# Optimization experiments

Measured on AMD Instinct MI355X. Metric: run time of the kernel, lower is better.

## Reference

```python
import jax, jax.numpy as jnp
import numpy as np

N_NODES = 100000
N_EDGES = 1280000
D_IN = 64
D_HID = 64
D_OUT = 1
N_GRAPHS = 512


def setup_inputs() -> dict:
    key = jax.random.key(0)
    ks = jax.random.split(key, 12)
    x = jax.random.normal(ks[0], (N_NODES, D_IN), dtype=jnp.float32)
    edge_index = jax.random.randint(ks[1], (2, N_EDGES), 0, N_NODES, dtype=jnp.int32)
    batch = jnp.sort(jax.random.randint(ks[2], (N_NODES,), 0, N_GRAPHS, dtype=jnp.int32))
    s = 0.1
    w0 = jax.random.normal(ks[3], (D_IN, D_HID), dtype=jnp.float32) * s
    b0 = jnp.zeros((D_HID,), dtype=jnp.float32)
    w1 = jax.random.normal(ks[4], (D_HID, D_HID), dtype=jnp.float32) * s
    b1 = jnp.zeros((D_HID,), dtype=jnp.float32)
    w2 = jax.random.normal(ks[5], (D_HID, D_HID), dtype=jnp.float32) * s
    b2 = jnp.zeros((D_HID,), dtype=jnp.float32)
    fc_w = jax.random.normal(ks[6], (D_HID, D_OUT), dtype=jnp.float32) * s
    fc_b = jnp.zeros((D_OUT,), dtype=jnp.float32)
    return {"x": x, "edge_index": edge_index, "batch": batch,
            "w0": w0, "b0": b0, "w1": w1, "b1": b1, "w2": w2, "b2": b2,
            "fc_w": fc_w, "fc_b": fc_b}


def _gcn_conv(x, w, b, src, dst):
    # PyG GCNConv: h = x @ W; out_i = sum_j norm_ij * h_j over (A + I), sym norm.
    h = x @ w                                           # [N, H]
    ones = jnp.ones((src.shape[0],), dtype=h.dtype)
    deg = jax.ops.segment_sum(ones, dst, num_segments=N_NODES) + 1.0  # +1 self-loop
    dinv = jax.lax.rsqrt(deg)                           # [N]
    norm = dinv[src] * dinv[dst]                        # [E]
    agg = jax.ops.segment_sum(h[src] * norm[:, None], dst, num_segments=N_NODES)
    agg = agg + h * (dinv * dinv)[:, None]              # self-loop term
    return agg + b


def reference(x, edge_index, batch, w0, b0, w1, b1, w2, b2, fc_w, fc_b):
    src, dst = edge_index[0], edge_index[1]
    # 3 stacked GCNConv + relu (dropout is identity in eval mode)
    h = jax.nn.relu(_gcn_conv(x, w0, b0, src, dst))
    h = jax.nn.relu(_gcn_conv(h, w1, b1, src, dst))
    h = jax.nn.relu(_gcn_conv(h, w2, b2, src, dst))
    # global mean pool per graph
    sums = jax.ops.segment_sum(h, batch, num_segments=N_GRAPHS)        # [G, H]
    cnt = jax.ops.segment_sum(jnp.ones((N_NODES,), h.dtype), batch, num_segments=N_GRAPHS)
    mean = sums / jnp.maximum(cnt, 1.0)[:, None]
    return mean @ fc_w + fc_b                            # [G, 1]
```

## Files before the change

kernel.cpp:

```cpp
#include <hip/hip_runtime.h>
#include <hip/hip_fp16.h>
#include <type_traits>

#define N_NODES 100000
#define N_EDGES 1280000
#define N_GRAPHS 512
#define NBK 196
#define CHUNK 3200
#define NCH 400
#define CAP 8192

typedef _Float16 v8h __attribute__((ext_vector_type(8)));
typedef float v4f __attribute__((ext_vector_type(4)));

__device__ inline void fmix_lo(float& acc, unsigned h2, float n) {
    asm volatile("v_fma_mix_f32 %0, %1, %2, %0 op_sel:[0,0,0] op_sel_hi:[1,0,0]"
                 : "+v"(acc) : "v"(h2), "v"(n));
}
__device__ inline void fmix_hi(float& acc, unsigned h2, float n) {
    asm volatile("v_fma_mix_f32 %0, %1, %2, %0 op_sel:[1,0,0] op_sel_hi:[1,0,0]"
                 : "+v"(acc) : "v"(h2), "v"(n));
}


__global__ __launch_bounds__(256) void edge_scatter(const int* __restrict__ src,
                                                    const int* __restrict__ dst,
                                                    int* __restrict__ bcur,
                                                    int2* __restrict__ pairs) {
    __shared__ int2 buf[CHUNK];
    __shared__ int lcnt[NBK], lloc[NBK], lcur[NBK];
    __shared__ int s[256];
    int t = threadIdx.x;
    for (int k = t; k < NBK; k += 256) { lcnt[k] = 0; lcur[k] = 0; }
    __syncthreads();
    int e0 = blockIdx.x * CHUNK;
    for (int i = t; i < CHUNK; i += 256) atomicAdd(&lcnt[dst[e0 + i] >> 9], 1);
    __syncthreads();
    {
        int v = (t < NBK) ? lcnt[t] : 0;
        s[t] = v; __syncthreads();
        for (int d = 1; d < 256; d <<= 1) {
            int x = (t >= d) ? s[t - d] : 0;
            __syncthreads();
            s[t] += x;
            __syncthreads();
        }
        if (t < NBK) lloc[t] = s[t] - v;
    }
    __syncthreads();
    for (int i = t; i < CHUNK; i += 256) {
        int d = dst[e0 + i];
        int k = d >> 9;
        int li = lloc[k] + atomicAdd(&lcur[k], 1);
        buf[li] = make_int2(src[e0 + i], d);
    }
    __syncthreads();
    for (int k = t; k < NBK; k += 256) {
        int c = lcnt[k];
        if (c) {
            int g = atomicAdd(&bcur[k * 16], c);
            int lo = lloc[k];
            int2* dstp = pairs + (size_t)k * CAP;
            for (int j = 0; j < c; j++)
                if (g + j < CAP) dstp[g + j] = buf[lo + j];
        }
    }
}


__global__ void bucket_scan(const int* __restrict__ bcur, int* __restrict__ bbase,
                            int* __restrict__ offs) {
    __shared__ int s[256];
    int t = threadIdx.x;
    int v = (t < NBK) ? min(bcur[t * 16], CAP) : 0;
    s[t] = v; __syncthreads();
    for (int d = 1; d < 256; d <<= 1) {
        int x = (t >= d) ? s[t - d] : 0;
        __syncthreads();
        s[t] += x;
        __syncthreads();
    }
    if (t < NBK) bbase[t] = s[t] - v;
    if (t == 0) offs[N_NODES] = N_EDGES;
}


__global__ __launch_bounds__(512) void bucket_place(const int2* __restrict__ pairs,
                                                    const int* __restrict__ bbase,
                                                    const int* __restrict__ bcur,
                                                    int* __restrict__ offs,
                                                    float* __restrict__ dinv,
                                                    int* __restrict__ csr) {
    __shared__ int lcnt[512];
    __shared__ int lofs[512];
    __shared__ int lcur[512];
    __shared__ int lsrc[CAP];
    int t = threadIdx.x;
    int b = blockIdx.x;
    int node0 = b << 9;
    int nn = min(512, N_NODES - node0);
    int beg = bbase[b];
    int cnt = min(bcur[b * 16], CAP);
    const int2* prs = pairs + (size_t)b * CAP;
    lcnt[t] = 0; lcur[t] = 0;
    __syncthreads();
    for (int i = t; i < cnt; i += 512)
        atomicAdd(&lcnt[prs[i].y - node0], 1);
    __syncthreads();
    int deg = lcnt[t];
    for (int d = 1; d < 512; d <<= 1) {
        int x = (t >= d) ? lcnt[t - d] : 0;
        __syncthreads();
        lcnt[t] += x;
        __syncthreads();
    }
    lofs[t] = lcnt[t] - deg;
    if (t < nn) {
        offs[node0 + t] = beg + lcnt[t] - deg;
        dinv[node0 + t] = 1.0f / sqrtf((float)deg + 1.0f);
    }
    __syncthreads();
    for (int i = t; i < cnt; i += 512) {
        int2 pr = prs[i];
        int n = pr.y - node0;
        int li = lofs[n] + atomicAdd(&lcur[n], 1);
        if (li < CAP) lsrc[li] = pr.x;
    }
    __syncthreads();
    for (int j = t; j < cnt; j += 512) csr[beg + j] = lsrc[j];
}


template <typename T>
__global__ __launch_bounds__(256) void gemm_mfma(const T* __restrict__ X,
                                                 const float* __restrict__ W,
                                                 __half* __restrict__ H) {
    __shared__ _Float16 Wt[64][72];
    int t = threadIdx.x;
    {
        #pragma unroll
        for (int q = 0; q < 4; q++) {
            int idx = t + q * 256;
            int k = idx >> 4;
            int n0 = (idx & 15) * 4;
            float4 v = ((const float4*)W)[idx];
            Wt[n0 + 0][k] = (_Float16)v.x;
            Wt[n0 + 1][k] = (_Float16)v.y;
            Wt[n0 + 2][k] = (_Float16)v.z;
            Wt[n0 + 3][k] = (_Float16)v.w;
        }
    }
    __syncthreads();

    int wv = t >> 6, lane = t & 63;
    int m = lane & 15, quad = lane >> 4;

    v8h bf[4][2];
    #pragma unroll
    for (int c = 0; c < 4; c++)
        #pragma unroll
        for (int h = 0; h < 2; h++)
            bf[c][h] = *(const v8h*)&Wt[c * 16 + m][h * 32 + quad * 8];

    int base = blockIdx.x * 256 + wv * 64;
    #pragma unroll
    for (int tt = 0; tt < 4; tt++) {
        int tile = base + tt * 16;
        int rA = min(tile + m, N_NODES - 1);
        v8h a0, a1;
        if constexpr (std::is_same<T, float>::value) {
            const float* xp = (const float*)X + (size_t)rA * 64 + quad * 8;
            float4 p0 = *(const float4*)xp;
            float4 p1 = *(const float4*)(xp + 4);
            float4 p2 = *(const float4*)(xp + 32);
            float4 p3 = *(const float4*)(xp + 36);
            a0 = (v8h){(_Float16)p0.x, (_Float16)p0.y, (_Float16)p0.z, (_Float16)p0.w,
                       (_Float16)p1.x, (_Float16)p1.y, (_Float16)p1.z, (_Float16)p1.w};
            a1 = (v8h){(_Float16)p2.x, (_Float16)p2.y, (_Float16)p2.z, (_Float16)p2.w,
                       (_Float16)p3.x, (_Float16)p3.y, (_Float16)p3.z, (_Float16)p3.w};
        } else {
            const _Float16* xp = (const _Float16*)X + (size_t)rA * 64 + quad * 8;
            a0 = *(const v8h*)xp;
            a1 = *(const v8h*)(xp + 32);
        }
        v4f acc[4];
        #pragma unroll
        for (int c = 0; c < 4; c++) {
            acc[c] = (v4f){0.f, 0.f, 0.f, 0.f};
            acc[c] = __builtin_amdgcn_mfma_f32_16x16x32_f16(a0, bf[c][0], acc[c], 0, 0, 0);
            acc[c] = __builtin_amdgcn_mfma_f32_16x16x32_f16(a1, bf[c][1], acc[c], 0, 0, 0);
        }
        #pragma unroll
        for (int r = 0; r < 4; r++) {
            int row = tile + quad * 4 + r;
            if (row < N_NODES) {
                __half* hp = H + (size_t)row * 64 + m;
                #pragma unroll
                for (int c = 0; c < 4; c++)
                    hp[c * 16] = __float2half(acc[c][r]);
            }
        }
    }
}


__device__ inline void agg_body(const uint2* __restrict__ Hh, int wid, int lane,
                                const int* __restrict__ offs,
                                const int* __restrict__ csr,
                                const float* __restrict__ dinv,
                                float4& out) {
    int eg = lane >> 4;
    int fq = lane & 15;
    int beg = offs[wid], end = offs[wid + 1];
    float di = dinv[wid];
    uint2 us = Hh[(size_t)wid * 16 + fq];

    float4 a0 = {0.f, 0.f, 0.f, 0.f};
    float4 a1 = {0.f, 0.f, 0.f, 0.f};
    for (int base = beg; base < end; base += 16) {
        int i0 = base + eg;
        int r0 = csr[i0], r1 = csr[i0 + 4], r2 = csr[i0 + 8], r3 = csr[i0 + 12];
        bool p0 = i0      < end, p1 = i0 + 4  < end,
             p2 = i0 + 8  < end, p3 = i0 + 12 < end;
        int s0 = p0 ? r0 : 0, s1 = p1 ? r1 : 0,
            s2 = p2 ? r2 : 0, s3 = p3 ? r3 : 0;
        uint2 u0 = Hh[(size_t)s0 * 16 + fq];
        uint2 u1 = Hh[(size_t)s1 * 16 + fq];
        uint2 u2 = Hh[(size_t)s2 * 16 + fq];
        uint2 u3 = Hh[(size_t)s3 * 16 + fq];
        float d0 = dinv[s0], d1 = dinv[s1], d2 = dinv[s2], d3 = dinv[s3];
        float n0 = p0 ? d0 * di : 0.f;
        float n1 = p1 ? d1 * di : 0.f;
        float n2 = p2 ? d2 * di : 0.f;
        float n3 = p3 ? d3 * di : 0.f;
        fmix_lo(a0.x, u0.x, n0); fmix_hi(a0.y, u0.x, n0);
        fmix_lo(a0.z, u0.y, n0); fmix_hi(a0.w, u0.y, n0);
        fmix_lo(a1.x, u1.x, n1); fmix_hi(a1.y, u1.x, n1);
        fmix_lo(a1.z, u1.y, n1); fmix_hi(a1.w, u1.y, n1);
        fmix_lo(a0.x, u2.x, n2); fmix_hi(a0.y, u2.x, n2);
        fmix_lo(a0.z, u2.y, n2); fmix_hi(a0.w, u2.y, n2);
        fmix_lo(a1.x, u3.x, n3); fmix_hi(a1.y, u3.x, n3);
        fmix_lo(a1.z, u3.y, n3); fmix_hi(a1.w, u3.y, n3);
    }
    a0.x += a1.x; a0.y += a1.y; a0.z += a1.z; a0.w += a1.w;
    a0.x += __shfl_xor(a0.x, 16); a0.y += __shfl_xor(a0.y, 16);
    a0.z += __shfl_xor(a0.z, 16); a0.w += __shfl_xor(a0.w, 16);
    a0.x += __shfl_xor(a0.x, 32); a0.y += __shfl_xor(a0.y, 32);
    a0.z += __shfl_xor(a0.z, 32); a0.w += __shfl_xor(a0.w, 32);
    float2 s01 = __half22float2(*(__half2*)&us.x);
    float2 s23 = __half22float2(*(__half2*)&us.y);
    float dd = di * di;
    out.x = a0.x + s01.x * dd; out.y = a0.y + s01.y * dd;
    out.z = a0.z + s23.x * dd; out.w = a0.w + s23.y * dd;
}

__global__ __launch_bounds__(256) void agg_gcn(const __half* __restrict__ H,
                                               const int* __restrict__ offs,
                                               const int* __restrict__ csr,
                                               const float* __restrict__ dinv,
                                               const float* __restrict__ bias,
                                               __half* __restrict__ Out) {
    int wid = (blockIdx.x * 256 + threadIdx.x) >> 6;
    int lane = threadIdx.x & 63;
    if (wid >= N_NODES) return;
    float4 r;
    agg_body((const uint2*)H, wid, lane, offs, csr, dinv, r);
    int fq = lane & 15;
    if ((lane >> 4) == 0) {
        float4 b4 = ((const float4*)bias)[fq];
        __half2 h01 = __float22half2_rn(make_float2(fmaxf(r.x + b4.x, 0.f),
                                                    fmaxf(r.y + b4.y, 0.f)));
        __half2 h23 = __float22half2_rn(make_float2(fmaxf(r.z + b4.z, 0.f),
                                                    fmaxf(r.w + b4.w, 0.f)));
        uint2 u;
        u.x = *(unsigned int*)&h01;
        u.y = *(unsigned int*)&h23;
        ((uint2*)Out)[(size_t)wid * 16 + fq] = u;
    }
}

__global__ __launch_bounds__(256) void agg_gcn_pool(const __half* __restrict__ H,
                                                    const int* __restrict__ offs,
                                                    const int* __restrict__ csr,
                                                    const float* __restrict__ dinv,
                                                    const float* __restrict__ bias,
                                                    const float* __restrict__ fcw,
                                                    float* __restrict__ p) {
    int wid = (blockIdx.x * 256 + threadIdx.x) >> 6;
    int lane = threadIdx.x & 63;
    if (wid >= N_NODES) return;
    float4 r;
    agg_body((const uint2*)H, wid, lane, offs, csr, dinv, r);
    int fq = lane & 15;
    float4 b4 = ((const float4*)bias)[fq];
    float4 f4 = ((const float4*)fcw)[fq];
    float v = fmaxf(r.x + b4.x, 0.f) * f4.x + fmaxf(r.y + b4.y, 0.f) * f4.y
            + fmaxf(r.z + b4.z, 0.f) * f4.z + fmaxf(r.w + b4.w, 0.f) * f4.w;
    v += __shfl_xor(v, 1); v += __shfl_xor(v, 2);
    v += __shfl_xor(v, 4); v += __shfl_xor(v, 8);
    if (lane == 0) p[wid] = v;
}


__device__ inline int lower_bound_batch(const int* __restrict__ batch, int key) {
    int lo = 0, hi = N_NODES;
    while (lo < hi) {
        int mid = (lo + hi) >> 1;
        if (batch[mid] < key) lo = mid + 1; else hi = mid;
    }
    return lo;
}

__global__ __launch_bounds__(256) void graph_reduce(const float* __restrict__ p,
                                                    const int* __restrict__ batch,
                                                    const float* __restrict__ fcb,
                                                    float* __restrict__ out) {
    __shared__ float red[4];
    int g = blockIdx.x;
    int s0 = lower_bound_batch(batch, g);
    int s1 = lower_bound_batch(batch, g + 1);
    float acc = 0.f;
    for (int i = s0 + threadIdx.x; i < s1; i += 256) acc += p[i];
    #pragma unroll
    for (int o = 32; o > 0; o >>= 1) acc += __shfl_xor(acc, o);
    int lane = threadIdx.x & 63, wv = threadIdx.x >> 6;
    if (lane == 0) red[wv] = acc;
    __syncthreads();
    if (threadIdx.x == 0) {
        float sum = red[0] + red[1] + red[2] + red[3];
        out[g] = sum / fmaxf((float)(s1 - s0), 1.f) + fcb[0];
    }
}


extern "C" void kernel_launch(void* const* d_in, const int* in_sizes, int n_in,
                              void* d_out, int out_size, void* d_ws, size_t ws_size,
                              hipStream_t stream) {
    const float* x    = (const float*)d_in[0];
    const int*   ei   = (const int*)d_in[1];
    const int*   batch= (const int*)d_in[2];
    const float* w0   = (const float*)d_in[3];
    const float* b0   = (const float*)d_in[4];
    const float* w1   = (const float*)d_in[5];
    const float* b1   = (const float*)d_in[6];
    const float* w2   = (const float*)d_in[7];
    const float* b2   = (const float*)d_in[8];
    const float* fcw  = (const float*)d_in[9];
    const float* fcb  = (const float*)d_in[10];
    float* out = (float*)d_out;

    const int* src_e = ei;
    const int* dst_e = ei + N_EDGES;

    char* w = (char*)d_ws;
    size_t o = 0;
    int*    bcur  = (int*)(w + o);    o += 256 * 16 * 4;
    int*    bbase = (int*)(w + o);    o += 256 * 4;
    int*    offs  = (int*)(w + o);    o += (size_t)(N_NODES + 8) * 4;
    float*  dinv  = (float*)(w + o);  o += (size_t)N_NODES * 4;
    int2*   pairs = (int2*)(w + o);   o += (size_t)NBK * CAP * 8;
    int*    csr   = (int*)(w + o);    o += (size_t)(N_EDGES + 16) * 4;
    __half* bufA  = (__half*)(w + o); o += (size_t)N_NODES * 64 * 2;
    __half* bufB  = (__half*)(w + o); o += (size_t)N_NODES * 64 * 2;
    float*  pvec  = (float*)(w + o);  o += (size_t)N_NODES * 4;

    hipMemsetAsync(bcur, 0, 256 * 16 * 4, stream);
    hipMemsetAsync(csr + N_EDGES, 0, 16 * 4, stream);

    edge_scatter<<<NCH, 256, 0, stream>>>(src_e, dst_e, bcur, pairs);
    bucket_scan<<<1, 256, 0, stream>>>(bcur, bbase, offs);
    bucket_place<<<NBK, 512, 0, stream>>>(pairs, bbase, bcur, offs, dinv, csr);

    const int GEMM_BLOCKS = (N_NODES + 255) / 256;
    const int AGG_BLOCKS  = (N_NODES + 3) / 4;

    gemm_mfma<float><<<GEMM_BLOCKS, 256, 0, stream>>>(x, w0, bufA);
    agg_gcn<<<AGG_BLOCKS, 256, 0, stream>>>(bufA, offs, csr, dinv, b0, bufB);

    gemm_mfma<__half><<<GEMM_BLOCKS, 256, 0, stream>>>(bufB, w1, bufA);
    agg_gcn<<<AGG_BLOCKS, 256, 0, stream>>>(bufA, offs, csr, dinv, b1, bufB);

    gemm_mfma<__half><<<GEMM_BLOCKS, 256, 0, stream>>>(bufB, w2, bufA);
    agg_gcn_pool<<<AGG_BLOCKS, 256, 0, stream>>>(bufA, offs, csr, dinv, b2, fcw, pvec);

    graph_reduce<<<N_GRAPHS, 256, 0, stream>>>(pvec, batch, fcb, out);
}
```

Baseline: 295.7 us.

## Fold source-side dinv into GEMM output and pre-scale CSR indices

The GEMM epilogue now multiplies each output row by dinv[row], so the aggregation no longer gathers dinv for every neighbor and only scales by the destination's dinv. CSR entries are stored pre-shifted by 4 so neighbor row offsets need no multiply and use 32-bit indexing. This drops one random gather per edge in each of the three aggregation layers. The cost is an extra dinv load in the GEMM epilogue and fp16 rounding of the prescaled values.

```diff
diff --git a/kernel.cpp b/kernel.cpp
--- a/kernel.cpp
+++ b/kernel.cpp
@@ -124,7 +124,7 @@
         int2 pr = prs[i];
         int n = pr.y - node0;
         int li = lofs[n] + atomicAdd(&lcur[n], 1);
-        if (li < CAP) lsrc[li] = pr.x;
+        if (li < CAP) lsrc[li] = pr.x << 4;
     }
     __syncthreads();
     for (int j = t; j < cnt; j += 512) csr[beg + j] = lsrc[j];
@@ -134,6 +134,7 @@
 template <typename T>
 __global__ __launch_bounds__(256) void gemm_mfma(const T* __restrict__ X,
                                                  const float* __restrict__ W,
+                                                 const float* __restrict__ dinv,
                                                  __half* __restrict__ H) {
     __shared__ _Float16 Wt[64][72];
     int t = threadIdx.x;
@@ -194,10 +195,11 @@
         for (int r = 0; r < 4; r++) {
             int row = tile + quad * 4 + r;
             if (row < N_NODES) {
+                float dv = dinv[row];
                 __half* hp = H + (size_t)row * 64 + m;
                 #pragma unroll
                 for (int c = 0; c < 4; c++)
-                    hp[c * 16] = __float2half(acc[c][r]);
+                    hp[c * 16] = __float2half(acc[c][r] * dv);
             }
         }
     }
@@ -213,7 +215,7 @@
     int fq = lane & 15;
     int beg = offs[wid], end = offs[wid + 1];
     float di = dinv[wid];
-    uint2 us = Hh[(size_t)wid * 16 + fq];
+    uint2 us = Hh[wid * 16 + fq];
 
     float4 a0 = {0.f, 0.f, 0.f, 0.f};
     float4 a1 = {0.f, 0.f, 0.f, 0.f};
@@ -224,15 +226,14 @@
              p2 = i0 + 8  < end, p3 = i0 + 12 < end;
         int s0 = p0 ? r0 : 0, s1 = p1 ? r1 : 0,
             s2 = p2 ? r2 : 0, s3 = p3 ? r3 : 0;
-        uint2 u0 = Hh[(size_t)s0 * 16 + fq];
-        uint2 u1 = Hh[(size_t)s1 * 16 + fq];
-        uint2 u2 = Hh[(size_t)s2 * 16 + fq];
-        uint2 u3 = Hh[(size_t)s3 * 16 + fq];
-        float d0 = dinv[s0], d1 = dinv[s1], d2 = dinv[s2], d3 = dinv[s3];
-        float n0 = p0 ? d0 * di : 0.f;
-        float n1 = p1 ? d1 * di : 0.f;
-        float n2 = p2 ? d2 * di : 0.f;
-        float n3 = p3 ? d3 * di : 0.f;
+        uint2 u0 = Hh[s0 + fq];
+        uint2 u1 = Hh[s1 + fq];
+        uint2 u2 = Hh[s2 + fq];
+        uint2 u3 = Hh[s3 + fq];
+        float n0 = p0 ? di : 0.f;
+        float n1 = p1 ? di : 0.f;
+        float n2 = p2 ? di : 0.f;
+        float n3 = p3 ? di : 0.f;
         fmix_lo(a0.x, u0.x, n0); fmix_hi(a0.y, u0.x, n0);
         fmix_lo(a0.z, u0.y, n0); fmix_hi(a0.w, u0.y, n0);
         fmix_lo(a1.x, u1.x, n1); fmix_hi(a1.y, u1.x, n1);
@@ -249,9 +250,8 @@
     a0.z += __shfl_xor(a0.z, 32); a0.w += __shfl_xor(a0.w, 32);
     float2 s01 = __half22float2(*(__half2*)&us.x);
     float2 s23 = __half22float2(*(__half2*)&us.y);
-    float dd = di * di;
-    out.x = a0.x + s01.x * dd; out.y = a0.y + s01.y * dd;
-    out.z = a0.z + s23.x * dd; out.w = a0.w + s23.y * dd;
+    out.x = a0.x + s01.x * di; out.y = a0.y + s01.y * di;
+    out.z = a0.z + s23.x * di; out.w = a0.w + s23.y * di;
 }
 
 __global__ __launch_bounds__(256) void agg_gcn(const __half* __restrict__ H,
@@ -374,13 +374,13 @@
     const int GEMM_BLOCKS = (N_NODES + 255) / 256;
     const int AGG_BLOCKS  = (N_NODES + 3) / 4;
 
-    gemm_mfma<float><<<GEMM_BLOCKS, 256, 0, stream>>>(x, w0, bufA);
+    gemm_mfma<float><<<GEMM_BLOCKS, 256, 0, stream>>>(x, w0, dinv, bufA);
     agg_gcn<<<AGG_BLOCKS, 256, 0, stream>>>(bufA, offs, csr, dinv, b0, bufB);
 
-    gemm_mfma<__half><<<GEMM_BLOCKS, 256, 0, stream>>>(bufB, w1, bufA);
+    gemm_mfma<__half><<<GEMM_BLOCKS, 256, 0, stream>>>(bufB, w1, dinv, bufA);
     agg_gcn<<<AGG_BLOCKS, 256, 0, stream>>>(bufA, offs, csr, dinv, b1, bufB);
 
-    gemm_mfma<__half><<<GEMM_BLOCKS, 256, 0, stream>>>(bufB, w2, bufA);
+    gemm_mfma<__half><<<GEMM_BLOCKS, 256, 0, stream>>>(bufB, w2, dinv, bufA);
     agg_gcn_pool<<<AGG_BLOCKS, 256, 0, stream>>>(bufA, offs, csr, dinv, b2, fcw, pvec);
 
     graph_reduce<<<N_GRAPHS, 256, 0, stream>>>(pvec, batch, fcb, out);
```

Result: no change. 295.9 us (+0.1%).
